# Kernel optimization log

Hardware: AMD Instinct MI355X
Metric: run time of the kernel (lower is better)

The kernel has to match this reference:

```python
import jax, jax.numpy as jnp
import numpy as np

TGT, SRC, BH, D = 2048, 2048, 16, 64

def setup_inputs() -> dict:
    key = jax.random.key(0)
    kq, kk, kv, km = jax.random.split(key, 4)
    return {
        "query": jax.random.normal(kq, (TGT, BH, D), dtype=jnp.float32),
        "key": jax.random.normal(kk, (SRC, BH, D), dtype=jnp.float32),
        "value": jax.random.normal(kv, (SRC, BH, D), dtype=jnp.float32),
        "attn_mask": jax.random.randint(km, (1, TGT, SRC), 0, 2).astype(jnp.bool_),
    }

def reference(query, key, value, attn_mask):
    # seq-first layout: [len, batch_heads, head_dim] -> [bh, len, d]
    head_dim = query.shape[-1]
    q = jnp.swapaxes(query, 0, 1) * (float(head_dim) ** -0.5)  # [bh, tgt, d]
    k = jnp.swapaxes(key, 0, 1)                                # [bh, src, d]
    v = jnp.swapaxes(value, 0, 1)                              # [bh, src, d]
    w = jnp.einsum('btd,bsd->bts', q, k)                       # [bh, tgt, src]
    w = jnp.where(attn_mask, jnp.float32(-1e8), w)
    w = jax.nn.softmax(w, axis=-1)
    # dropout p=0.0 (eval) -> identity
    out = jnp.einsum('bts,bsd->btd', w, v)                     # [bh, tgt, d]
    return jnp.swapaxes(out, 0, 1), w  # ([tgt, bh, d], [bh, tgt, src])
```

## Files before the change

kernel.cpp:

```cpp
#include <hip/hip_runtime.h>

#define TGT 2048
#define SRC 2048
#define BH 16
#define HD 64
#define BT 16
#define SROW 2056

typedef __bf16 bf16x8 __attribute__((ext_vector_type(8)));
typedef unsigned short ushortx8 __attribute__((ext_vector_type(8)));
typedef float floatx4 __attribute__((ext_vector_type(4)));

__device__ int g_mask_is_u8;

__device__ __forceinline__ unsigned short f2bf(float f) {
  unsigned u = __builtin_bit_cast(unsigned, f);
  u += 0x7FFFu + ((u >> 16) & 1u);
  return (unsigned short)(u >> 16);
}
__device__ __forceinline__ float bf2f(unsigned short s) {
  unsigned u = ((unsigned)s) << 16;
  return __builtin_bit_cast(float, u);
}

__global__ void detect_mask_fmt(const unsigned char* __restrict__ m) {
  __shared__ int any;
  if (threadIdx.x == 0) any = 0;
  __syncthreads();
  int local = 0;
  int base = threadIdx.x * 16;
#pragma unroll
  for (int i = 0; i < 16; ++i) {
    int idx = base + i;
    if (idx & 3) local |= m[idx];
  }
  if (local) atomicOr(&any, 1);
  __syncthreads();
  if (threadIdx.x == 0) g_mask_is_u8 = (any != 0);
}

__global__ void cvt_qk(const float* __restrict__ q, const float* __restrict__ k,
                       unsigned short* __restrict__ qb, unsigned short* __restrict__ kb) {
  const int gid = blockIdx.x * 256 + threadIdx.x;
  const int half = TGT * BH * HD / 8;
  const float* src; unsigned short* dst; float sc;
  int idx;
  if (gid < half) { src = q; dst = qb; sc = 0.125f; idx = gid; }
  else            { src = k; dst = kb; sc = 1.0f;  idx = gid - half; }
  const float* p = src + (size_t)idx * 8;
  float4 a = *(const float4*)p;
  float4 b = *(const float4*)(p + 4);
  union { unsigned short u[8]; ushortx8 v; } o;
  o.u[0] = f2bf(a.x * sc); o.u[1] = f2bf(a.y * sc);
  o.u[2] = f2bf(a.z * sc); o.u[3] = f2bf(a.w * sc);
  o.u[4] = f2bf(b.x * sc); o.u[5] = f2bf(b.y * sc);
  o.u[6] = f2bf(b.z * sc); o.u[7] = f2bf(b.w * sc);
  *(ushortx8*)(dst + (size_t)idx * 8) = o.v;
}

__global__ void v_tr(const float* __restrict__ v, unsigned short* __restrict__ vt) {
  __shared__ unsigned short tile[64 * 72];
  const int h = blockIdx.x >> 5;
  const int s0 = (blockIdx.x & 31) * 64;
  const int tid = threadIdx.x;
  const int sr = tid >> 4, c = tid & 15;
#pragma unroll
  for (int p = 0; p < 4; ++p) {
    const int s = sr + p * 16;
    float4 f = *(const float4*)(v + (size_t)(s0 + s) * (BH * HD) + h * HD + c * 4);
    tile[(c * 4 + 0) * 72 + s] = f2bf(f.x);
    tile[(c * 4 + 1) * 72 + s] = f2bf(f.y);
    tile[(c * 4 + 2) * 72 + s] = f2bf(f.z);
    tile[(c * 4 + 3) * 72 + s] = f2bf(f.w);
  }
  __syncthreads();
  const int d = tid >> 2, q4 = tid & 3;
  ushortx8 o0 = *(const ushortx8*)&tile[d * 72 + q4 * 16];
  ushortx8 o1 = *(const ushortx8*)&tile[d * 72 + q4 * 16 + 8];
  unsigned short* dst = vt + (size_t)h * HD * SRC + (size_t)d * SRC + s0 + q4 * 16;
  *(ushortx8*)dst = o0;
  *(ushortx8*)(dst + 8) = o1;
}

__launch_bounds__(512, 2)
__global__ void attn_kernel(const unsigned short* __restrict__ qb,
                            const unsigned short* __restrict__ kb,
                            const unsigned short* __restrict__ vtb,
                            const unsigned char* __restrict__ mask8,
                            const int* __restrict__ mask32,
                            float* __restrict__ out0,
                            float* __restrict__ wout) {
  extern __shared__ char smem[];
  unsigned short* smS = (unsigned short*)smem;
  float* redArr = (float*)(smem + BT * SROW * 2);
  float* rowmaxArr = redArr + 1024;
  float* invArr = rowmaxArr + BT;

  const int bid = blockIdx.x;
  const int h = bid >> 7;
  const int t0 = (bid & 127) * BT;
  const int tid = threadIdx.x;
  const int wv = tid >> 6;
  const int lane = tid & 63;
  const int quad = lane >> 4;
  const int l16 = lane & 15;
  const bool is_u8 = (g_mask_is_u8 != 0);

  bf16x8 aq[2];
  {
    const unsigned short* qp = qb + (size_t)(t0 + l16) * (BH * HD) + h * HD + quad * 8;
    aq[0] = __builtin_bit_cast(bf16x8, *(const ushortx8*)qp);
    aq[1] = __builtin_bit_cast(bf16x8, *(const ushortx8*)(qp + 32));
  }

  for (int st = wv; st < SRC / 16; st += 8) {
    const int sbase = st * 16;
    const unsigned short* kp = kb + (size_t)(sbase + l16) * (BH * HD) + h * HD + quad * 8;
    bf16x8 bk0 = __builtin_bit_cast(bf16x8, *(const ushortx8*)kp);
    bf16x8 bk1 = __builtin_bit_cast(bf16x8, *(const ushortx8*)(kp + 32));
    floatx4 c = {0.f, 0.f, 0.f, 0.f};
    c = __builtin_amdgcn_mfma_f32_16x16x32_bf16(aq[0], bk0, c, 0, 0, 0);
    c = __builtin_amdgcn_mfma_f32_16x16x32_bf16(aq[1], bk1, c, 0, 0, 0);
    const int scol = sbase + l16;
#pragma unroll
    for (int r = 0; r < 4; ++r) {
      const int tl = quad * 4 + r;
      const float val = c[r];
      const float oth = __shfl_xor(val, 1);
      if (!(l16 & 1)) {
        unsigned pk2 = (unsigned)f2bf(val) | ((unsigned)f2bf(oth) << 16);
        *(unsigned*)&smS[tl * SROW + scol] = pk2;
      }
    }
  }
  __syncthreads();

  {
    const int row = tid >> 5;
    const int cc = tid & 31;
    unsigned short* srow = smS + row * SROW;
    const size_t mbase = (size_t)(t0 + row) * SRC;
    float pmax = -3.4e38f;
#pragma unroll
    for (int kk = 0; kk < 8; ++kk) {
      const int col = cc * 8 + kk * 256;
      ushortx8 u = *(const ushortx8*)&srow[col];
      unsigned mbits[8];
      if (is_u8) {
        uint2 m2 = *(const uint2*)(mask8 + mbase + col);
#pragma unroll
        for (int i = 0; i < 4; ++i) { mbits[i] = (m2.x >> (8 * i)) & 0xFF; mbits[4 + i] = (m2.y >> (8 * i)) & 0xFF; }
      } else {
        const int4 a = *(const int4*)(mask32 + mbase + col);
        const int4 b = *(const int4*)(mask32 + mbase + col + 4);
        mbits[0] = a.x; mbits[1] = a.y; mbits[2] = a.z; mbits[3] = a.w;
        mbits[4] = b.x; mbits[5] = b.y; mbits[6] = b.z; mbits[7] = b.w;
      }
      union { unsigned short u[8]; ushortx8 v; } o;
#pragma unroll
      for (int i = 0; i < 8; ++i) {
        float val = mbits[i] ? -1e8f : bf2f(u[i]);
        pmax = fmaxf(pmax, val);
        o.u[i] = f2bf(val);
      }
      *(ushortx8*)&srow[col] = o.v;
    }
    redArr[row * 32 + cc] = pmax;
  }
  __syncthreads();
  if (tid < BT) {
    float m = -3.4e38f;
    for (int j = 0; j < 32; ++j) m = fmaxf(m, redArr[tid * 32 + j]);
    rowmaxArr[tid] = m;
  }
  __syncthreads();

  {
    const int row = tid >> 5;
    const int cc = tid & 31;
    const float rm = rowmaxArr[row];
    unsigned short* srow = smS + row * SROW;
    float psum = 0.f;
#pragma unroll
    for (int kk = 0; kk < 8; ++kk) {
      const int col = cc * 8 + kk * 256;
      ushortx8 u = *(const ushortx8*)&srow[col];
      union { unsigned short u[8]; ushortx8 v; } o;
#pragma unroll
      for (int i = 0; i < 8; ++i) {
        float e = __expf(bf2f(u[i]) - rm);
        psum += e;
        o.u[i] = f2bf(e);
      }
      *(ushortx8*)&srow[col] = o.v;
    }
    redArr[row * 32 + cc] = psum;
  }
  __syncthreads();
  if (tid < BT) {
    float s = 0.f;
    for (int j = 0; j < 32; ++j) s += redArr[tid * 32 + j];
    invArr[tid] = 1.0f / s;
  }
  __syncthreads();

  {
    const int row = tid >> 5;
    const int cc = tid & 31;
    const float invv = invArr[row];
    float* wrow = wout + ((size_t)h * TGT + (t0 + row)) * SRC;
    const unsigned short* srow = smS + row * SROW;
#pragma unroll
    for (int kk = 0; kk < 8; ++kk) {
      const int col = cc * 8 + kk * 256;
      ushortx8 u = *(const ushortx8*)&srow[col];
      float4 a, b;
      a.x = bf2f(u[0]) * invv; a.y = bf2f(u[1]) * invv;
      a.z = bf2f(u[2]) * invv; a.w = bf2f(u[3]) * invv;
      b.x = bf2f(u[4]) * invv; b.y = bf2f(u[5]) * invv;
      b.z = bf2f(u[6]) * invv; b.w = bf2f(u[7]) * invv;
      *(float4*)&wrow[col] = a;
      *(float4*)&wrow[col + 4] = b;
    }
  }

  {
    const int dt = wv & 3;
    const int halfsel = wv >> 2;
    const int dbase = dt * 16;
    const int sstart = halfsel * 1024;
    const unsigned short* vp = vtb + (size_t)h * HD * SRC +
                               (size_t)(dbase + l16) * SRC + sstart + quad * 8;
    const unsigned short* sp = smS + l16 * SROW + sstart + quad * 8;
    floatx4 acc = {0.f, 0.f, 0.f, 0.f};
    for (int s0 = 0; s0 < 1024; s0 += 32) {
      bf16x8 af = __builtin_bit_cast(bf16x8, *(const ushortx8*)(sp + s0));
      bf16x8 bfv = __builtin_bit_cast(bf16x8, *(const ushortx8*)(vp + s0));
      acc = __builtin_amdgcn_mfma_f32_16x16x32_bf16(af, bfv, acc, 0, 0, 0);
    }
    if (halfsel) {
#pragma unroll
      for (int r = 0; r < 4; ++r)
        redArr[dt * 256 + (quad * 4 + r) * 16 + l16] = acc[r];
    }
    __syncthreads();
    if (!halfsel) {
#pragma unroll
      for (int r = 0; r < 4; ++r) {
        const int tl = quad * 4 + r;
        float s = acc[r] + redArr[dt * 256 + tl * 16 + l16];
        out0[((size_t)(t0 + tl) * BH + h) * HD + dbase + l16] = s * invArr[tl];
      }
    }
  }
}

extern "C" void kernel_launch(void* const* d_in, const int* in_sizes, int n_in,
                              void* d_out, int out_size, void* d_ws, size_t ws_size,
                              hipStream_t stream) {
  const float* q = (const float*)d_in[0];
  const float* k = (const float*)d_in[1];
  const float* v = (const float*)d_in[2];
  const unsigned char* m8 = (const unsigned char*)d_in[3];
  const int* m32 = (const int*)d_in[3];
  float* out0 = (float*)d_out;
  float* wout = out0 + (size_t)TGT * BH * HD;

  unsigned short* qb = (unsigned short*)d_ws;
  unsigned short* kb = qb + (size_t)TGT * BH * HD;
  unsigned short* vt = kb + (size_t)SRC * BH * HD;

  const size_t shbytes = (size_t)BT * SROW * 2 + 1024 * 4 + BT * 4 + BT * 4;
  hipFuncSetAttribute((const void*)attn_kernel,
                      hipFuncAttributeMaxDynamicSharedMemorySize, (int)shbytes);

  detect_mask_fmt<<<1, 256, 0, stream>>>(m8);
  cvt_qk<<<dim3(2048), dim3(256), 0, stream>>>(q, k, qb, kb);
  v_tr<<<dim3(BH * (SRC / 64)), dim3(256), 0, stream>>>(v, vt);
  attn_kernel<<<dim3(BH * (TGT / BT)), dim3(512), shbytes, stream>>>(
      qb, kb, vt, m8, m32, out0, wout);
}
```

Measured before the change: 432.1 us.

## Keep attention scores in registers and merge prep kernels into one launch

Masking, row max, exp and row sum are now done on the QK^T MFMA results held in registers, using shuffle reductions across the 16-lane groups. This replaces three full read-modify-write passes over the shared-memory score tile, and the tile is now written only once, with the final probabilities. The three preprocessing kernels (mask format detection, Q/K conversion, V transpose) are merged into a single launch to save launch overhead. In exchange, the mask and weight output are accessed as scalar per-element loads and stores instead of vectors, which weakens coalescing. Launch bounds are raised to 4 blocks per CU, which lowers the register budget and risks spilling the 32-entry packed array.

```diff
diff --git a/kernel.cpp b/kernel.cpp
--- a/kernel.cpp
+++ b/kernel.cpp
@@ -23,66 +23,67 @@
   return __builtin_bit_cast(float, u);
 }
 
-__global__ void detect_mask_fmt(const unsigned char* __restrict__ m) {
+__global__ void prep(const float* __restrict__ q, const float* __restrict__ k,
+                     const float* __restrict__ v, const unsigned char* __restrict__ m,
+                     unsigned short* __restrict__ qb, unsigned short* __restrict__ kb,
+                     unsigned short* __restrict__ vt) {
+  __shared__ unsigned short tile[64 * 72];
   __shared__ int any;
-  if (threadIdx.x == 0) any = 0;
-  __syncthreads();
-  int local = 0;
-  int base = threadIdx.x * 16;
-#pragma unroll
-  for (int i = 0; i < 16; ++i) {
-    int idx = base + i;
-    if (idx & 3) local |= m[idx];
-  }
-  if (local) atomicOr(&any, 1);
-  __syncthreads();
-  if (threadIdx.x == 0) g_mask_is_u8 = (any != 0);
-}
-
-__global__ void cvt_qk(const float* __restrict__ q, const float* __restrict__ k,
-                       unsigned short* __restrict__ qb, unsigned short* __restrict__ kb) {
-  const int gid = blockIdx.x * 256 + threadIdx.x;
-  const int half = TGT * BH * HD / 8;
-  const float* src; unsigned short* dst; float sc;
-  int idx;
-  if (gid < half) { src = q; dst = qb; sc = 0.125f; idx = gid; }
-  else            { src = k; dst = kb; sc = 1.0f;  idx = gid - half; }
-  const float* p = src + (size_t)idx * 8;
-  float4 a = *(const float4*)p;
-  float4 b = *(const float4*)(p + 4);
-  union { unsigned short u[8]; ushortx8 v; } o;
-  o.u[0] = f2bf(a.x * sc); o.u[1] = f2bf(a.y * sc);
-  o.u[2] = f2bf(a.z * sc); o.u[3] = f2bf(a.w * sc);
-  o.u[4] = f2bf(b.x * sc); o.u[5] = f2bf(b.y * sc);
-  o.u[6] = f2bf(b.z * sc); o.u[7] = f2bf(b.w * sc);
-  *(ushortx8*)(dst + (size_t)idx * 8) = o.v;
-}
-
-__global__ void v_tr(const float* __restrict__ v, unsigned short* __restrict__ vt) {
-  __shared__ unsigned short tile[64 * 72];
-  const int h = blockIdx.x >> 5;
-  const int s0 = (blockIdx.x & 31) * 64;
+  const int b = blockIdx.x;
   const int tid = threadIdx.x;
-  const int sr = tid >> 4, c = tid & 15;
-#pragma unroll
-  for (int p = 0; p < 4; ++p) {
-    const int s = sr + p * 16;
-    float4 f = *(const float4*)(v + (size_t)(s0 + s) * (BH * HD) + h * HD + c * 4);
-    tile[(c * 4 + 0) * 72 + s] = f2bf(f.x);
-    tile[(c * 4 + 1) * 72 + s] = f2bf(f.y);
-    tile[(c * 4 + 2) * 72 + s] = f2bf(f.z);
-    tile[(c * 4 + 3) * 72 + s] = f2bf(f.w);
-  }
-  __syncthreads();
-  const int d = tid >> 2, q4 = tid & 3;
-  ushortx8 o0 = *(const ushortx8*)&tile[d * 72 + q4 * 16];
-  ushortx8 o1 = *(const ushortx8*)&tile[d * 72 + q4 * 16 + 8];
-  unsigned short* dst = vt + (size_t)h * HD * SRC + (size_t)d * SRC + s0 + q4 * 16;
-  *(ushortx8*)dst = o0;
-  *(ushortx8*)(dst + 8) = o1;
-}
-
-__launch_bounds__(512, 2)
+  if (b < 2048) {
+    const int gid = b * 256 + tid;
+    const int half = TGT * BH * HD / 8;
+    const float* src; unsigned short* dst; float sc; int idx;
+    if (gid < half) { src = q; dst = qb; sc = 0.125f; idx = gid; }
+    else            { src = k; dst = kb; sc = 1.0f;  idx = gid - half; }
+    const float* p = src + (size_t)idx * 8;
+    float4 a = *(const float4*)p;
+    float4 bb = *(const float4*)(p + 4);
+    union { unsigned short u[8]; ushortx8 v; } o;
+    o.u[0] = f2bf(a.x * sc); o.u[1] = f2bf(a.y * sc);
+    o.u[2] = f2bf(a.z * sc); o.u[3] = f2bf(a.w * sc);
+    o.u[4] = f2bf(bb.x * sc); o.u[5] = f2bf(bb.y * sc);
+    o.u[6] = f2bf(bb.z * sc); o.u[7] = f2bf(bb.w * sc);
+    *(ushortx8*)(dst + (size_t)idx * 8) = o.v;
+  } else if (b < 2560) {
+    const int bb = b - 2048;
+    const int h = bb >> 5;
+    const int s0 = (bb & 31) * 64;
+    const int sr = tid >> 4, c = tid & 15;
+#pragma unroll
+    for (int p = 0; p < 4; ++p) {
+      const int s = sr + p * 16;
+      float4 f = *(const float4*)(v + (size_t)(s0 + s) * (BH * HD) + h * HD + c * 4);
+      tile[(c * 4 + 0) * 72 + s] = f2bf(f.x);
+      tile[(c * 4 + 1) * 72 + s] = f2bf(f.y);
+      tile[(c * 4 + 2) * 72 + s] = f2bf(f.z);
+      tile[(c * 4 + 3) * 72 + s] = f2bf(f.w);
+    }
+    __syncthreads();
+    const int d = tid >> 2, q4 = tid & 3;
+    ushortx8 o0 = *(const ushortx8*)&tile[d * 72 + q4 * 16];
+    ushortx8 o1 = *(const ushortx8*)&tile[d * 72 + q4 * 16 + 8];
+    unsigned short* dst = vt + (size_t)h * HD * SRC + (size_t)d * SRC + s0 + q4 * 16;
+    *(ushortx8*)dst = o0;
+    *(ushortx8*)(dst + 8) = o1;
+  } else {
+    if (tid == 0) any = 0;
+    __syncthreads();
+    int local = 0;
+    int base = tid * 16;
+#pragma unroll
+    for (int i = 0; i < 16; ++i) {
+      int idx = base + i;
+      if (idx & 3) local |= m[idx];
+    }
+    if (local) atomicOr(&any, 1);
+    __syncthreads();
+    if (tid == 0) g_mask_is_u8 = (any != 0);
+  }
+}
+
+__launch_bounds__(512, 4)
 __global__ void attn_kernel(const unsigned short* __restrict__ qb,
                             const unsigned short* __restrict__ kb,
                             const unsigned short* __restrict__ vtb,
@@ -113,7 +114,11 @@
     aq[1] = __builtin_bit_cast(bf16x8, *(const ushortx8*)(qp + 32));
   }
 
-  for (int st = wv; st < SRC / 16; st += 8) {
+  float rmax[4] = {-3.4e38f, -3.4e38f, -3.4e38f, -3.4e38f};
+  unsigned pk[32];
+#pragma unroll
+  for (int ki = 0; ki < 16; ++ki) {
+    const int st = wv + ki * 8;
     const int sbase = st * 16;
     const unsigned short* kp = kb + (size_t)(sbase + l16) * (BH * HD) + h * HD + quad * 8;
     bf16x8 bk0 = __builtin_bit_cast(bf16x8, *(const ushortx8*)kp);
@@ -124,105 +129,86 @@
     const int scol = sbase + l16;
 #pragma unroll
     for (int r = 0; r < 4; ++r) {
-      const int tl = quad * 4 + r;
-      const float val = c[r];
-      const float oth = __shfl_xor(val, 1);
-      if (!(l16 & 1)) {
-        unsigned pk2 = (unsigned)f2bf(val) | ((unsigned)f2bf(oth) << 16);
-        *(unsigned*)&smS[tl * SROW + scol] = pk2;
-      }
-    }
-  }
-  __syncthreads();
-
-  {
-    const int row = tid >> 5;
-    const int cc = tid & 31;
-    unsigned short* srow = smS + row * SROW;
-    const size_t mbase = (size_t)(t0 + row) * SRC;
-    float pmax = -3.4e38f;
-#pragma unroll
-    for (int kk = 0; kk < 8; ++kk) {
-      const int col = cc * 8 + kk * 256;
-      ushortx8 u = *(const ushortx8*)&srow[col];
-      unsigned mbits[8];
-      if (is_u8) {
-        uint2 m2 = *(const uint2*)(mask8 + mbase + col);
-#pragma unroll
-        for (int i = 0; i < 4; ++i) { mbits[i] = (m2.x >> (8 * i)) & 0xFF; mbits[4 + i] = (m2.y >> (8 * i)) & 0xFF; }
-      } else {
-        const int4 a = *(const int4*)(mask32 + mbase + col);
-        const int4 b = *(const int4*)(mask32 + mbase + col + 4);
-        mbits[0] = a.x; mbits[1] = a.y; mbits[2] = a.z; mbits[3] = a.w;
-        mbits[4] = b.x; mbits[5] = b.y; mbits[6] = b.z; mbits[7] = b.w;
-      }
-      union { unsigned short u[8]; ushortx8 v; } o;
-#pragma unroll
-      for (int i = 0; i < 8; ++i) {
-        float val = mbits[i] ? -1e8f : bf2f(u[i]);
-        pmax = fmaxf(pmax, val);
-        o.u[i] = f2bf(val);
-      }
-      *(ushortx8*)&srow[col] = o.v;
-    }
-    redArr[row * 32 + cc] = pmax;
+      const size_t midx = (size_t)(t0 + quad * 4 + r) * SRC + scol;
+      const int mv = is_u8 ? (int)mask8[midx] : mask32[midx];
+      const float val = mv ? -1e8f : c[r];
+      rmax[r] = fmaxf(rmax[r], val);
+      const unsigned bb = (unsigned)f2bf(val);
+      const int pi = (ki >> 1) * 4 + r;
+      if (ki & 1) pk[pi] |= (bb << 16); else pk[pi] = bb;
+    }
+  }
+
+#pragma unroll
+  for (int off = 1; off < 16; off <<= 1)
+#pragma unroll
+    for (int r = 0; r < 4; ++r) rmax[r] = fmaxf(rmax[r], __shfl_xor(rmax[r], off));
+  if (l16 == 0) {
+#pragma unroll
+    for (int r = 0; r < 4; ++r) redArr[(quad * 4 + r) * 8 + wv] = rmax[r];
   }
   __syncthreads();
   if (tid < BT) {
-    float m = -3.4e38f;
-    for (int j = 0; j < 32; ++j) m = fmaxf(m, redArr[tid * 32 + j]);
+    float m = redArr[tid * 8];
+#pragma unroll
+    for (int j = 1; j < 8; ++j) m = fmaxf(m, redArr[tid * 8 + j]);
     rowmaxArr[tid] = m;
   }
   __syncthreads();
 
-  {
-    const int row = tid >> 5;
-    const int cc = tid & 31;
-    const float rm = rowmaxArr[row];
-    unsigned short* srow = smS + row * SROW;
-    float psum = 0.f;
-#pragma unroll
-    for (int kk = 0; kk < 8; ++kk) {
-      const int col = cc * 8 + kk * 256;
-      ushortx8 u = *(const ushortx8*)&srow[col];
-      union { unsigned short u[8]; ushortx8 v; } o;
-#pragma unroll
-      for (int i = 0; i < 8; ++i) {
-        float e = __expf(bf2f(u[i]) - rm);
-        psum += e;
-        o.u[i] = f2bf(e);
-      }
-      *(ushortx8*)&srow[col] = o.v;
-    }
-    redArr[row * 32 + cc] = psum;
+  float rsum[4] = {0.f, 0.f, 0.f, 0.f};
+  {
+    float rm[4];
+#pragma unroll
+    for (int r = 0; r < 4; ++r) rm[r] = rowmaxArr[quad * 4 + r];
+#pragma unroll
+    for (int pi = 0; pi < 32; ++pi) {
+      const int r = pi & 3;
+      const unsigned p = pk[pi];
+      const float e0 = __expf(bf2f((unsigned short)(p & 0xFFFF)) - rm[r]);
+      const float e1 = __expf(bf2f((unsigned short)(p >> 16)) - rm[r]);
+      rsum[r] += e0 + e1;
+      pk[pi] = (unsigned)f2bf(e0) | ((unsigned)f2bf(e1) << 16);
+    }
+  }
+#pragma unroll
+  for (int off = 1; off < 16; off <<= 1)
+#pragma unroll
+    for (int r = 0; r < 4; ++r) rsum[r] += __shfl_xor(rsum[r], off);
+  if (l16 == 0) {
+#pragma unroll
+    for (int r = 0; r < 4; ++r) redArr[(quad * 4 + r) * 8 + wv] = rsum[r];
   }
   __syncthreads();
   if (tid < BT) {
     float s = 0.f;
-    for (int j = 0; j < 32; ++j) s += redArr[tid * 32 + j];
+#pragma unroll
+    for (int j = 0; j < 8; ++j) s += redArr[tid * 8 + j];
     invArr[tid] = 1.0f / s;
   }
   __syncthreads();
 
   {
-    const int row = tid >> 5;
-    const int cc = tid & 31;
-    const float invv = invArr[row];
-    float* wrow = wout + ((size_t)h * TGT + (t0 + row)) * SRC;
-    const unsigned short* srow = smS + row * SROW;
-#pragma unroll
-    for (int kk = 0; kk < 8; ++kk) {
-      const int col = cc * 8 + kk * 256;
-      ushortx8 u = *(const ushortx8*)&srow[col];
-      float4 a, b;
-      a.x = bf2f(u[0]) * invv; a.y = bf2f(u[1]) * invv;
-      a.z = bf2f(u[2]) * invv; a.w = bf2f(u[3]) * invv;
-      b.x = bf2f(u[4]) * invv; b.y = bf2f(u[5]) * invv;
-      b.z = bf2f(u[6]) * invv; b.w = bf2f(u[7]) * invv;
-      *(float4*)&wrow[col] = a;
-      *(float4*)&wrow[col + 4] = b;
-    }
-  }
+    float iv[4];
+#pragma unroll
+    for (int r = 0; r < 4; ++r) iv[r] = invArr[quad * 4 + r];
+#pragma unroll
+    for (int pi = 0; pi < 32; ++pi) {
+      const int r = pi & 3;
+      const int pair = pi >> 2;
+      const int col0 = wv * 16 + pair * 256 + l16;
+      const unsigned p = pk[pi];
+      const unsigned short b0 = (unsigned short)(p & 0xFFFF);
+      const unsigned short b1 = (unsigned short)(p >> 16);
+      float* wr = wout + ((size_t)h * TGT + t0 + quad * 4 + r) * SRC;
+      wr[col0] = bf2f(b0) * iv[r];
+      wr[col0 + 128] = bf2f(b1) * iv[r];
+      unsigned short* sr = smS + (quad * 4 + r) * SROW;
+      sr[col0] = b0;
+      sr[col0 + 128] = b1;
+    }
+  }
+  __syncthreads();
 
   {
     const int dt = wv & 3;
@@ -274,9 +260,7 @@
   hipFuncSetAttribute((const void*)attn_kernel,
                       hipFuncAttributeMaxDynamicSharedMemorySize, (int)shbytes);
 
-  detect_mask_fmt<<<1, 256, 0, stream>>>(m8);
-  cvt_qk<<<dim3(2048), dim3(256), 0, stream>>>(q, k, qb, kb);
-  v_tr<<<dim3(BH * (SRC / 64)), dim3(256), 0, stream>>>(v, vt);
+  prep<<<dim3(2561), dim3(256), 0, stream>>>(q, k, v, m8, qb, kb, vt);
   attn_kernel<<<dim3(BH * (TGT / BT)), dim3(512), shbytes, stream>>>(
       qb, kb, vt, m8, m32, out0, wout);
 }
```

Measured after the change: 459.4 us. 1.06x slower.
